# Kernel tuning notes

Hardware: AMD Instinct MI355X
Metric: run time of the kernel (lower is better)

## Reference

```python
import jax, jax.numpy as jnp
import numpy as np

# Perfect 8-ary tree, 6 levels, level-order node indexing.
K = 8            # children per internal node
D = 512          # embedding_dim
P = 8            # number of dependency types (num_params)
OFF = [0, 1, 9, 73, 585, 4681, 37449]  # level start offsets; N = 37449
N = OFF[-1]


def setup_inputs() -> dict:
    key = jax.random.key(0)
    ks = jax.random.split(key, 8)
    s = 1.0 / np.sqrt(D)  # torch default-ish init scale, avoids LSTM saturation
    return {
        "embeddings": jax.random.normal(ks[0], (N, D), dtype=jnp.float32),
        "dep_types": jax.random.randint(ks[1], (N,), 0, P, dtype=jnp.int32),
        "W_dep": jax.random.normal(ks[2], (P, D, D), dtype=jnp.float32) * s,
        "b_dep": jax.random.normal(ks[3], (P, D), dtype=jnp.float32) * s,
        "W_ih": jax.random.normal(ks[4], (4 * D, D), dtype=jnp.float32) * s,
        "W_hh": jax.random.normal(ks[5], (4 * D, D), dtype=jnp.float32) * s,
        "b_ih": jax.random.normal(ks[6], (4 * D,), dtype=jnp.float32) * s,
        "b_hh": jax.random.normal(ks[7], (4 * D,), dtype=jnp.float32) * s,
    }


def _lstm_final_c(seq, W_ih, W_hh, b_ih, b_hh):
    # seq: [B, T, D]; 1-layer LSTM with zero init state; returns final cell state c_T [B, D]
    B = seq.shape[0]
    h0 = jnp.zeros((B, D), seq.dtype)

    def step(carry, z_t):
        h, c = carry
        gates = z_t @ W_ih.T + h @ W_hh.T + b_ih + b_hh  # [B, 4D]
        i, f, g, o = jnp.split(gates, 4, axis=-1)        # torch gate order i,f,g,o
        i, f, o = jax.nn.sigmoid(i), jax.nn.sigmoid(f), jax.nn.sigmoid(o)
        g = jnp.tanh(g)
        c = f * c + i * g
        h = o * jnp.tanh(c)
        return (h, c), None

    (h, c), _ = jax.lax.scan(step, (h0, h0), jnp.swapaxes(seq, 0, 1))
    return c


def reference(embeddings, dep_types, W_dep, b_dep, W_ih, W_hh, b_ih, b_hh):
    # Leaves (level 5): LSTM over length-1 sequence [x] -> final cell state.
    leaf_x = embeddings[OFF[5]:OFF[6]]                       # [32768, D]
    z = _lstm_final_c(leaf_x[:, None, :], W_ih, W_hh, b_ih, b_hh)

    # Level-synchronous bottom-up sweep (exactly the recursion's per-node math).
    for l in range(4, -1, -1):
        m = OFF[l + 1] - OFF[l]                              # nodes at this level
        child_z = z.reshape(m, K, D)                         # children's subtree codes
        child_dep = dep_types[OFF[l + 1]:OFF[l + 2]].reshape(m, K)
        onehot = jax.nn.one_hot(child_dep, P, dtype=child_z.dtype)  # [m, K, P]
        # per-dep Linear: z_c = W_dep[dep] @ x_c + b_dep[dep]
        zc = jnp.einsum('mkj,pij,mkp->mki', child_z, W_dep, onehot) + onehot @ b_dep
        x = embeddings[OFF[l]:OFF[l + 1]]                    # node's own embedding, last in seq
        seq = jnp.concatenate([zc, x[:, None, :]], axis=1)   # [m, K+1, D]
        z = _lstm_final_c(seq, W_ih, W_hh, b_ih, b_hh)

    return z  # root sentence embedding, [1, D]
```

## Files before the change

### kernel.cpp

```cpp
#include <hip/hip_runtime.h>

typedef __attribute__((ext_vector_type(8))) short short8;
typedef __attribute__((ext_vector_type(4))) float f32x4;
typedef _Float16 half_t;

__device__ __forceinline__ unsigned short f2bf(float x){
  union { float f; unsigned u; } v; v.f = x;
  unsigned r = v.u + 0x7fffu + ((v.u >> 16) & 1u);
  return (unsigned short)(r >> 16);
}
__device__ __forceinline__ float sigm(float x){ return 1.0f / (1.0f + __expf(-x)); }
__device__ __forceinline__ float tanh_(float x){
  float e = __expf(2.0f * x);
  return 1.0f - 2.0f / (e + 1.0f);
}
__device__ __forceinline__ short8 load_bf8_f32(const float* p){
  float4 a = *(const float4*)p;
  float4 b = *(const float4*)(p + 4);
  short8 r;
  r[0]=(short)f2bf(a.x); r[1]=(short)f2bf(a.y); r[2]=(short)f2bf(a.z); r[3]=(short)f2bf(a.w);
  r[4]=(short)f2bf(b.x); r[5]=(short)f2bf(b.y); r[6]=(short)f2bf(b.z); r[7]=(short)f2bf(b.w);
  return r;
}
__device__ __forceinline__ f32x4 mfma16(short8 a, short8 b, f32x4 c){
  return __builtin_amdgcn_mfma_f32_16x16x32_bf16(a, b, c, 0, 0, 0);
}
__device__ __forceinline__ void gload16(const void* g, void* lds){
  __builtin_amdgcn_global_load_lds((const __attribute__((address_space(1))) void*)g,
                                   (__attribute__((address_space(3))) void*)lds, 16, 0, 0);
}
__device__ __forceinline__ f32x4 shfl_xor4(f32x4 v, int m){
  f32x4 r;
  r[0]=__shfl_xor(v[0],m); r[1]=__shfl_xor(v[1],m);
  r[2]=__shfl_xor(v[2],m); r[3]=__shfl_xor(v[3],m);
  return r;
}
__device__ __forceinline__ float pick4(f32x4 v, int k){
  float a = (k&1)? v[1] : v[0];
  float b = (k&1)? v[3] : v[2];
  return (k&2)? b : a;
}
__device__ __forceinline__ f32x4 sel4(f32x4 a0, f32x4 a1, f32x4 a2, f32x4 a3, int k){
  f32x4 x = (k&1)? a1 : a0;
  f32x4 y = (k&1)? a3 : a2;
  return (k&2)? y : x;
}

#define KSTAGE1(AB, BB, off)                                                         \
  {                                                                                  \
    _Pragma("unroll")                                                                \
    for (int q = 0; q < 4; ++q){                                                     \
      gload16(AB[q] + (off), As + (q*32 + w*8)*64);                                  \
      gload16(BB[q] + (off), Bs + (q*32 + w*8)*64);                                  \
    }                                                                                \
  }

#define KCOMP1                                                                       \
  {                                                                                  \
    _Pragma("unroll")                                                                \
    for (int kk = 0; kk < 2; ++kk){                                                  \
      short8 av[4], bv[4];                                                           \
      _Pragma("unroll")                                                              \
      for (int i = 0; i < 4; ++i)                                                    \
        av[i] = *(const short8*)&As[(wm*64 + i*16 + r15)*64 + (((kk*4 + g4) ^ (r15 & 7))*8)]; \
      _Pragma("unroll")                                                              \
      for (int i = 0; i < 4; ++i)                                                    \
        bv[i] = *(const short8*)&Bs[(wn*64 + i*16 + r15)*64 + (((kk*4 + g4) ^ (r15 & 7))*8)]; \
      _Pragma("unroll")                                                              \
      for (int i = 0; i < 4; ++i)                                                    \
        _Pragma("unroll")                                                            \
        for (int j = 0; j < 4; ++j) acc[i][j] = mfma16(av[i], bv[j], acc[i][j]);     \
    }                                                                                \
  }

#define KLOOP1(AB, BB)                                                               \
  for (int kt = 0; kt < 8; ++kt){                                                    \
    KSTAGE1(AB, BB, kt*64)                                                           \
    __syncthreads();                                                                 \
    KCOMP1                                                                           \
    __syncthreads();                                                                 \
  }

__global__ __launch_bounds__(256) void prep_kernel(
    const float* __restrict__ emb, const int* __restrict__ dep,
    const float* __restrict__ W_dep, const float* __restrict__ b_dep,
    const float* __restrict__ W_ih, const float* __restrict__ W_hh,
    const float* __restrict__ b_ih, const float* __restrict__ b_hh,
    unsigned short* __restrict__ embb, unsigned short* __restrict__ Wih_il,
    unsigned short* __restrict__ Whh_il, unsigned short* __restrict__ Wleaf,
    unsigned short* __restrict__ WdT, float* __restrict__ bsum, float* __restrict__ bc,
    int* __restrict__ perm, int* __restrict__ tile_p, int* __restrict__ meta)
{
  const int bid = blockIdx.x, tid = threadIdx.x;
  if (bid < 1024){
    for (size_t i = (size_t)bid*256 + tid; i < 2396736ull; i += 1024ull*256)
      *(short8*)(embb + i*8) = load_bf8_f32(emb + i*8);
  } else if (bid < 1536){
    int idx = (bid-1024)*256 + tid; int r = idx >> 6, c8 = idx & 63;
    int sr = (r & 3)*512 + (r >> 2);
    *(short8*)(Wih_il + (size_t)r*512 + c8*8) = load_bf8_f32(W_ih + (size_t)sr*512 + c8*8);
  } else if (bid < 2048){
    int idx = (bid-1536)*256 + tid; int r = idx >> 6, c8 = idx & 63;
    int sr = (r & 3)*512 + (r >> 2);
    *(short8*)(Whh_il + (size_t)r*512 + c8*8) = load_bf8_f32(W_hh + (size_t)sr*512 + c8*8);
  } else if (bid < 2304){
    int idx = (bid-2048)*256 + tid; int r = idx >> 6, c8 = idx & 63;
    int sr = ((r & 1) ? 2 : 0)*512 + (r >> 1);
    *(short8*)(Wleaf + (size_t)r*512 + c8*8) = load_bf8_f32(W_ih + (size_t)sr*512 + c8*8);
  } else if (bid < 2816){
    __shared__ unsigned short tle[64][65];
    int lb = bid - 2304; int p = lb >> 6; int tile = lb & 63;
    int i0 = (tile >> 3)*64, j0 = (tile & 7)*64;
    const float* src = W_dep + (size_t)p*512*512;
    for (int q = 0; q < 16; ++q){
      int e = q*256 + tid; int li = e >> 6, lj = e & 63;
      tle[li][lj] = f2bf(src[(size_t)(i0+li)*512 + (j0+lj)]);
    }
    __syncthreads();
    unsigned short* dst = WdT + (size_t)p*512*512;
    for (int q = 0; q < 16; ++q){
      int e = q*256 + tid; int lj = e >> 6, li = e & 63;
      dst[(size_t)(j0+lj)*512 + (i0+li)] = tle[li][lj];
    }
  } else if (bid < 2824){
    int r = (bid-2816)*256 + tid;
    if (r < 2048){ int g = r & 3, j = r >> 2; bsum[r] = b_ih[g*512+j] + b_hh[g*512+j]; }
  } else if (bid < 2888){
    __shared__ float bd[512];
    int lb = bid - 2824; int p = lb >> 3, ch = lb & 7;
    for (int i = tid; i < 512; i += 256) bd[i] = b_dep[p*512 + i];
    __syncthreads();
    int r = ch*256 + tid; int g = r & 3, j = r >> 2;
    const float* wr = W_ih + (size_t)(g*512 + j)*512;
    float s = 0.0f;
    for (int i = 0; i < 512; ++i) s = fmaf(wr[i], bd[i], s);
    bc[(size_t)p*2048 + r] = s;
  } else {
    __shared__ int cnt[8], base[8], fill[8];
    int lb = bid - 2888; const int l = lb >> 3, t = lb & 7;
    const int M_[5]  = {1,8,64,512,4096};
    const int CB_[5] = {1,9,73,585,4681};
    const int MT_[5] = {8,8,8,12,40};
    const int PB_[5] = {69632,61440,53248,40960,0};
    const int TB_[5] = {544,480,416,320,0};
    const int m = M_[l], cb = CB_[l], MT = MT_[l];
    int* pm = perm + PB_[l] + t*MT*128;
    int* tp = tile_p + TB_[l] + t*MT;
    if (tid < 8){ cnt[tid] = 0; fill[tid] = 0; }
    __syncthreads();
    for (int n = tid; n < m; n += 256) atomicAdd(&cnt[dep[cb + n*8 + t]], 1);
    __syncthreads();
    if (tid == 0){
      int tiles = 0;
      for (int p = 0; p < 8; ++p){
        base[p] = tiles*128;
        int g = (cnt[p] + 127) >> 7;
        for (int q = 0; q < g; ++q) tp[tiles + q] = p;
        tiles += g;
      }
      meta[l*8 + t] = tiles;
    }
    __syncthreads();
    for (int i = tid; i < MT*128; i += 256) pm[i] = -1;
    __syncthreads();
    for (int n = tid; n < m; n += 256){
      int p = dep[cb + n*8 + t];
      pm[base[p] + atomicAdd(&fill[p], 1)] = n;
    }
  }
}

__global__ __launch_bounds__(256) void combo_gemm(
    const unsigned short* __restrict__ A,
    const unsigned short* __restrict__ WdT,
    unsigned short* __restrict__ C)
{
  const int p  = blockIdx.x >> 6;
  const int mt = (blockIdx.x >> 2) & 15;
  const int nb = blockIdx.x & 3;
  __shared__ unsigned short As[8192];
  __shared__ unsigned short Bs[8192];
  const int tid = threadIdx.x, lane = tid & 63, w = tid >> 6;
  const int wm = w >> 1, wn = w & 1;
  const int r15 = lane & 15, g4 = lane >> 4;
  const int kc = ((lane & 7) ^ (lane >> 3)) * 8;

  const unsigned short* ab[4]; const unsigned short* bb[4];
  #pragma unroll
  for (int q = 0; q < 4; ++q){
    int rl = mt*128 + q*32 + w*8 + (lane >> 3);
    ab[q] = A + (size_t)rl*512 + kc;
    int br = nb*128 + q*32 + w*8 + (lane >> 3);
    bb[q] = WdT + (size_t)p*262144 + (size_t)br*512 + kc;
  }
  f32x4 acc[4][4] = {};
  KLOOP1(ab, bb)
  unsigned short* Cp = C + (size_t)p*1048576;
  #pragma unroll
  for (int mi = 0; mi < 4; ++mi)
    #pragma unroll
    for (int ni = 0; ni < 4; ++ni)
      #pragma unroll
      for (int j = 0; j < 4; ++j){
        int row = mt*128 + wm*64 + mi*16 + g4*4 + j;
        int col = nb*128 + wn*64 + ni*16 + r15;
        Cp[(size_t)row*512 + col] = f2bf(acc[mi][ni][j]);
      }
}

__global__ __launch_bounds__(256) void leaf_gemm(
    const unsigned short* __restrict__ embL,
    const unsigned short* __restrict__ Wleaf,
    const float* __restrict__ bsum,
    unsigned short* __restrict__ zo)
{
  const int mt = (blockIdx.x & 7)*32 + ((blockIdx.x >> 3) & 31);
  const int nb = blockIdx.x >> 8;
  __shared__ unsigned short As[8192];
  __shared__ unsigned short Bs[8192];
  const int tid = threadIdx.x, lane = tid & 63, w = tid >> 6;
  const int wm = w >> 1, wn = w & 1;
  const int r15 = lane & 15, g4 = lane >> 4;
  const int kc = ((lane & 7) ^ (lane >> 3)) * 8;

  const unsigned short* ab[4]; const unsigned short* bb[4];
  #pragma unroll
  for (int q = 0; q < 4; ++q){
    int rl = mt*128 + q*32 + w*8 + (lane >> 3);
    ab[q] = embL + (size_t)rl*512 + kc;
    int br = nb*128 + q*32 + w*8 + (lane >> 3);
    bb[q] = Wleaf + (size_t)br*512 + kc;
  }
  f32x4 acc[4][4] = {};
  KLOOP1(ab, bb)
  const int g2 = r15 & 1;
  #pragma unroll
  for (int ni = 0; ni < 4; ++ni){
    int ci = nb*128 + wn*64 + ni*16 + r15;
    float b = bsum[4*(ci >> 1) + (g2 ? 2 : 0)];
    #pragma unroll
    for (int mi = 0; mi < 4; ++mi){
      acc[mi][ni][0]+=b; acc[mi][ni][1]+=b; acc[mi][ni][2]+=b; acc[mi][ni][3]+=b;
    }
  }
  #pragma unroll
  for (int mi = 0; mi < 4; ++mi)
    #pragma unroll
    for (int ni = 0; ni < 4; ++ni){
      f32x4 a0 = acc[mi][ni];
      f32x4 a1 = shfl_xor4(a0, 1);
      f32x4 vi_ = g2 ? a1 : a0;
      f32x4 vg_ = g2 ? a0 : a1;
      int jz = (nb*128 + wn*64 + ni*16 + r15) >> 1;
      #pragma unroll
      for (int u = 0; u < 2; ++u){
        int jrow = (g2 << 1) + u;
        float zi = pick4(vi_, jrow), zg = pick4(vg_, jrow);
        int row = mt*128 + wm*64 + mi*16 + g4*4 + jrow;
        zo[(size_t)row*512 + jz] = f2bf(sigm(zi) * tanh_(zg));
      }
    }
}

__device__ __forceinline__ void step_core(
    unsigned short* As, unsigned short* Bs,
    const unsigned short* __restrict__ embb,
    const unsigned short* __restrict__ Wcombo,
    const unsigned short* __restrict__ Wih_il,
    const unsigned short* __restrict__ Whh_il,
    const float* __restrict__ bsum, const float* __restrict__ bc,
    const unsigned short* __restrict__ zin, unsigned short* __restrict__ zo,
    const unsigned short* __restrict__ hi, unsigned short* __restrict__ ho,
    float* __restrict__ cbuf, float* __restrict__ outp,
    const int* __restrict__ pm, const int* __restrict__ tp,
    int node_base, int m, int t, int mt, int nbq, int l)
{
  const int tid = threadIdx.x, lane = tid & 63, w = tid >> 6;
  const int wm = w >> 1, wn = w & 1;
  const int r15 = lane & 15, g4 = lane >> 4;
  const int kc = ((lane & 7) ^ (lane >> 3)) * 8;
  const int first = (t == 0), last = (t == 8);
  const int p = tp ? tp[mt] : 0;

  int nn[4];
  #pragma unroll
  for (int q = 0; q < 4; ++q){
    int rl = mt*128 + q*32 + w*8 + (lane >> 3);
    int n = pm ? pm[rl] : (rl < m ? rl : -1);
    nn[q] = (n < 0) ? 0 : n;
  }
  f32x4 acc[4][4] = {};
  {
    const unsigned short* Bx = (t < 8) ? (Wcombo + (size_t)p*1048576) : Wih_il;
    const unsigned short* ab[4]; const unsigned short* bb[4];
    #pragma unroll
    for (int q = 0; q < 4; ++q){
      ab[q] = (t < 8) ? (zin + ((size_t)nn[q]*8 + t)*512 + kc)
                      : (embb + (size_t)(node_base + nn[q])*512 + kc);
      int br = nbq*128 + q*32 + w*8 + (lane >> 3);
      bb[q] = Bx + (size_t)br*512 + kc;
    }
    KLOOP1(ab, bb)
  }
  if (!first){
    const unsigned short* ab[4]; const unsigned short* bb[4];
    #pragma unroll
    for (int q = 0; q < 4; ++q){
      ab[q] = hi + (size_t)nn[q]*512 + kc;
      int br = nbq*128 + q*32 + w*8 + (lane >> 3);
      bb[q] = Whh_il + (size_t)br*512 + kc;
    }
    KLOOP1(ab, bb)
  }
  const int gate = r15 & 3;
  #pragma unroll
  for (int ni = 0; ni < 4; ++ni){
    int ci = nbq*128 + wn*64 + ni*16 + r15;
    float b = bsum[ci] + ((t < 8) ? bc[(size_t)p*2048 + ci] : 0.0f);
    #pragma unroll
    for (int mi = 0; mi < 4; ++mi){
      acc[mi][ni][0]+=b; acc[mi][ni][1]+=b; acc[mi][ni][2]+=b; acc[mi][ni][3]+=b;
    }
  }
  const int jr = r15 & 3;
  #pragma unroll
  for (int mi = 0; mi < 4; ++mi){
    int rl = mt*128 + wm*64 + mi*16 + g4*4 + jr;
    int n = pm ? pm[rl] : (rl < m ? rl : -1);
    #pragma unroll
    for (int ni = 0; ni < 4; ++ni){
      f32x4 a0 = acc[mi][ni];
      f32x4 a1 = shfl_xor4(a0, 1);
      f32x4 a2 = shfl_xor4(a0, 2);
      f32x4 a3 = shfl_xor4(a1, 2);
      f32x4 vi_ = sel4(a0,a1,a2,a3, gate);
      f32x4 vf_ = sel4(a0,a1,a2,a3, gate^1);
      f32x4 vg_ = sel4(a0,a1,a2,a3, gate^2);
      f32x4 vo_ = sel4(a0,a1,a2,a3, gate^3);
      float xi = pick4(vi_, jr), xf = pick4(vf_, jr);
      float xg = pick4(vg_, jr), xo = pick4(vo_, jr);
      if (n >= 0){
        int jz = nbq*32 + wn*16 + ni*4 + (r15 >> 2);
        size_t idx = (size_t)n*512 + jz;
        float i_ = sigm(xi), f_ = sigm(xf), g_ = tanh_(xg), o_ = sigm(xo);
        float cold = first ? 0.0f : cbuf[idx];
        float cn = fmaf(f_, cold, i_*g_);
        if (!last){ cbuf[idx] = cn; ho[idx] = f2bf(o_*tanh_(cn)); }
        else { if (l > 0) zo[idx] = f2bf(cn); else outp[idx] = cn; }
      }
    }
  }
}

__global__ __launch_bounds__(256) void step_kernel(
    const unsigned short* __restrict__ embb,
    const unsigned short* __restrict__ Wcombo,
    const unsigned short* __restrict__ Wih_il,
    const unsigned short* __restrict__ Whh_il,
    const float* __restrict__ bsum, const float* __restrict__ bc,
    const unsigned short* __restrict__ zin, unsigned short* __restrict__ zo,
    const unsigned short* __restrict__ hi, unsigned short* __restrict__ ho,
    float* __restrict__ cbuf, float* __restrict__ outp,
    const int* __restrict__ perm_t, const int* __restrict__ tile_t,
    const int* __restrict__ meta_t,
    int fixed_nt, int MTcap, int node_base, int m, int t, int l)
{
  __shared__ unsigned short As[8192];
  __shared__ unsigned short Bs[8192];
  int ntiles = meta_t ? *meta_t : fixed_nt;
  if (ntiles > MTcap) ntiles = MTcap;
  const int njobs = ntiles * 16;
  const int chunk = (njobs + 7) >> 3;
  const int g = blockIdx.x & 7, i = blockIdx.x >> 3;
  const int job = g*chunk + i;
  if (i >= chunk || job >= njobs) return;
  const int mt = job % ntiles, nbq = job / ntiles;
  step_core(As, Bs, embb, Wcombo, Wih_il, Whh_il, bsum, bc, zin, zo, hi, ho,
            cbuf, outp, perm_t, tile_t, node_base, m, t, mt, nbq, l);
}

__global__ __launch_bounds__(256) void gatex_kernel(
    const unsigned short* __restrict__ embb,
    const unsigned short* __restrict__ Wcombo,
    const unsigned short* __restrict__ Wih_il,
    const float* __restrict__ bsum, const float* __restrict__ bc,
    const unsigned short* __restrict__ zin,
    half_t* __restrict__ gx, unsigned short* __restrict__ h0out,
    float* __restrict__ cbuf,
    const int* __restrict__ perm_l, const int* __restrict__ tile_l,
    const int* __restrict__ meta_l,
    int MT, int m, int node_base)
{
  __shared__ unsigned short As[8192];
  __shared__ unsigned short Bs[8192];
  const int jt = blockIdx.x >> 4, nbq = blockIdx.x & 15;
  int t, mt, p = 0;
  const int* pm = nullptr;
  if (jt < 8*MT){
    t = jt / MT; mt = jt - t*MT;
    if (mt >= meta_l[t]) return;
    pm = perm_l + t*MT*128;
    p = tile_l[t*MT + mt];
  } else {
    t = 8; mt = jt - 8*MT;
  }
  const int tid = threadIdx.x, lane = tid & 63, w = tid >> 6;
  const int wm = w >> 1, wn = w & 1;
  const int r15 = lane & 15, g4 = lane >> 4;
  const int kc = ((lane & 7) ^ (lane >> 3)) * 8;

  int nn[4];
  #pragma unroll
  for (int q = 0; q < 4; ++q){
    int rl = mt*128 + q*32 + w*8 + (lane >> 3);
    int n = pm ? pm[rl] : (rl < m ? rl : -1);
    nn[q] = (n < 0) ? 0 : n;
  }
  const unsigned short* Bx = (t < 8) ? (Wcombo + (size_t)p*1048576) : Wih_il;
  const unsigned short* ab[4]; const unsigned short* bb[4];
  #pragma unroll
  for (int q = 0; q < 4; ++q){
    ab[q] = (t < 8) ? (zin + ((size_t)nn[q]*8 + t)*512 + kc)
                    : (embb + (size_t)(node_base + nn[q])*512 + kc);
    int br = nbq*128 + q*32 + w*8 + (lane >> 3);
    bb[q] = Bx + (size_t)br*512 + kc;
  }
  f32x4 acc[4][4] = {};
  KLOOP1(ab, bb)

  #pragma unroll
  for (int ni = 0; ni < 4; ++ni){
    int ci = nbq*128 + wn*64 + ni*16 + r15;
    float b = bsum[ci] + ((t < 8) ? bc[(size_t)p*2048 + ci] : 0.0f);
    #pragma unroll
    for (int mi = 0; mi < 4; ++mi){
      acc[mi][ni][0]+=b; acc[mi][ni][1]+=b; acc[mi][ni][2]+=b; acc[mi][ni][3]+=b;
    }
  }

  if (t == 0){
    const int gate = r15 & 3;
    const int jr = r15 & 3;
    #pragma unroll
    for (int mi = 0; mi < 4; ++mi){
      int rl = mt*128 + wm*64 + mi*16 + g4*4 + jr;
      int n = pm ? pm[rl] : (rl < m ? rl : -1);
      #pragma unroll
      for (int ni = 0; ni < 4; ++ni){
        f32x4 a0 = acc[mi][ni];
        f32x4 a1 = shfl_xor4(a0, 1);
        f32x4 a2 = shfl_xor4(a0, 2);
        f32x4 a3 = shfl_xor4(a1, 2);
        f32x4 vi_ = sel4(a0,a1,a2,a3, gate);
        f32x4 vg_ = sel4(a0,a1,a2,a3, gate^2);
        f32x4 vo_ = sel4(a0,a1,a2,a3, gate^3);
        float xi = pick4(vi_, jr);
        float xg = pick4(vg_, jr);
        float xo = pick4(vo_, jr);
        if (n >= 0){
          int jz = nbq*32 + wn*16 + ni*4 + (r15 >> 2);
          size_t idx = (size_t)n*512 + jz;
          float cn = sigm(xi) * tanh_(xg);
          cbuf[idx] = cn;
          h0out[idx] = f2bf(sigm(xo) * tanh_(cn));
        }
      }
    }
  } else {
    #pragma unroll
    for (int mi = 0; mi < 4; ++mi)
      #pragma unroll
      for (int ni = 0; ni < 4; ++ni){
        int ci = nbq*128 + wn*64 + ni*16 + r15;
        #pragma unroll
        for (int j = 0; j < 4; ++j){
          int rl = mt*128 + wm*64 + mi*16 + g4*4 + j;
          int n = pm ? pm[rl] : (rl < m ? rl : -1);
          if (n >= 0) gx[((size_t)t*m + n)*2048 + ci] = (half_t)acc[mi][ni][j];
        }
      }
  }
}

__global__ __launch_bounds__(256) void hstep_kernel(
    const unsigned short* __restrict__ Whh_il,
    const half_t* __restrict__ gx,
    const unsigned short* __restrict__ hi, unsigned short* __restrict__ ho,
    float* __restrict__ cbuf,
    unsigned short* __restrict__ zo, float* __restrict__ outp,
    int m, int t, int last)
{
  __shared__ unsigned short As[8192];
  __shared__ unsigned short Bs[8192];
  const int mt = blockIdx.x >> 4, nbq = blockIdx.x & 15;
  const int tid = threadIdx.x, lane = tid & 63, w = tid >> 6;
  const int wm = w >> 1, wn = w & 1;
  const int r15 = lane & 15, g4 = lane >> 4;
  const int kc = ((lane & 7) ^ (lane >> 3)) * 8;

  int nn[4];
  #pragma unroll
  for (int q = 0; q < 4; ++q){
    int rl = mt*128 + q*32 + w*8 + (lane >> 3);
    nn[q] = (rl < m) ? rl : 0;
  }
  const unsigned short* ab[4]; const unsigned short* bb[4];
  #pragma unroll
  for (int q = 0; q < 4; ++q){
    ab[q] = hi + (size_t)nn[q]*512 + kc;
    int br = nbq*128 + q*32 + w*8 + (lane >> 3);
    bb[q] = Whh_il + (size_t)br*512 + kc;
  }
  f32x4 acc[4][4] = {};
  KLOOP1(ab, bb)

  #pragma unroll
  for (int mi = 0; mi < 4; ++mi)
    #pragma unroll
    for (int ni = 0; ni < 4; ++ni){
      int ci = nbq*128 + wn*64 + ni*16 + r15;
      #pragma unroll
      for (int j = 0; j < 4; ++j){
        int rl = mt*128 + wm*64 + mi*16 + g4*4 + j;
        if (rl < m) acc[mi][ni][j] += (float)gx[((size_t)t*m + rl)*2048 + ci];
      }
    }

  const int gate = r15 & 3;
  const int jr = r15 & 3;
  #pragma unroll
  for (int mi = 0; mi < 4; ++mi){
    int rl = mt*128 + wm*64 + mi*16 + g4*4 + jr;
    int n = (rl < m) ? rl : -1;
    #pragma unroll
    for (int ni = 0; ni < 4; ++ni){
      f32x4 a0 = acc[mi][ni];
      f32x4 a1 = shfl_xor4(a0, 1);
      f32x4 a2 = shfl_xor4(a0, 2);
      f32x4 a3 = shfl_xor4(a1, 2);
      f32x4 vi_ = sel4(a0,a1,a2,a3, gate);
      f32x4 vf_ = sel4(a0,a1,a2,a3, gate^1);
      f32x4 vg_ = sel4(a0,a1,a2,a3, gate^2);
      f32x4 vo_ = sel4(a0,a1,a2,a3, gate^3);
      float xi = pick4(vi_, jr), xf = pick4(vf_, jr);
      float xg = pick4(vg_, jr), xo = pick4(vo_, jr);
      if (n >= 0){
        int jz = nbq*32 + wn*16 + ni*4 + (r15 >> 2);
        size_t idx = (size_t)n*512 + jz;
        float i_ = sigm(xi), f_ = sigm(xf), g_ = tanh_(xg), o_ = sigm(xo);
        float cn = fmaf(f_, cbuf[idx], i_*g_);
        if (!last){ cbuf[idx] = cn; ho[idx] = f2bf(o_*tanh_(cn)); }
        else { if (zo) zo[idx] = f2bf(cn); else outp[idx] = cn; }
      }
    }
  }
}

extern "C" void kernel_launch(void* const* d_in, const int* in_sizes, int n_in,
                              void* d_out, int out_size, void* d_ws, size_t ws_size,
                              hipStream_t stream)
{
  (void)in_sizes; (void)n_in; (void)out_size; (void)ws_size;
  const float* emb   = (const float*)d_in[0];
  const int*   dep   = (const int*)  d_in[1];
  const float* W_dep = (const float*)d_in[2];
  const float* b_dep = (const float*)d_in[3];
  const float* W_ih  = (const float*)d_in[4];
  const float* W_hh  = (const float*)d_in[5];
  const float* b_ih  = (const float*)d_in[6];
  const float* b_hh  = (const float*)d_in[7];
  float* out = (float*)d_out;

  unsigned short* embb   = (unsigned short*)d_ws;
  unsigned short* Wih_il = embb   + 19173888ull;
  unsigned short* Whh_il = Wih_il + 1048576ull;
  unsigned short* Wleaf  = Whh_il + 1048576ull;
  unsigned short* WdT    = Wleaf  + 524288ull;
  unsigned short* Wcombo = WdT    + 2097152ull;
  unsigned short* Z0     = Wcombo + 8388608ull;
  unsigned short* Z1     = Z0     + 16777216ull;
  unsigned short* hA     = Z1     + 2097152ull;
  unsigned short* hB     = hA     + 2097152ull;
  float* cbuf  = (float*)(hB + 2097152ull);
  float* bsum  = cbuf + 2097152ull;
  float* bc    = bsum + 2048;
  int*  perm   = (int*)(bc + 16384);
  int*  tile_p = perm + 77824;
  int*  meta   = tile_p + 608;
  half_t* gx   = (half_t*)(meta + 40);

  prep_kernel<<<2928, 256, 0, stream>>>(emb, dep, W_dep, b_dep, W_ih, W_hh, b_ih, b_hh,
                                        embb, Wih_il, Whh_il, Wleaf, WdT, bsum, bc,
                                        perm, tile_p, meta);
  combo_gemm<<<512, 256, 0, stream>>>(Wih_il, WdT, Wcombo);
  leaf_gemm<<<2048, 256, 0, stream>>>(embb + (size_t)4681*512, Wleaf, bsum, Z0);

  for (int t = 0; t <= 8; ++t){
    const unsigned short* hi = (t & 1) ? hA : hB;
    unsigned short* ho       = (t & 1) ? hB : hA;
    int grid = (t < 8) ? 40*16 : 32*16;
    step_kernel<<<grid, 256, 0, stream>>>(
        embb, Wcombo, Wih_il, Whh_il, bsum, bc,
        Z0, Z1, hi, ho, cbuf, nullptr,
        (t < 8) ? (perm + t*40*128) : nullptr,
        (t < 8) ? (tile_p + t*40) : nullptr,
        (t < 8) ? (meta + 4*8 + t) : nullptr,
        32, 40, 585, 4096, t, 4);
  }

  struct LvP { int m, MT, PB, TB, nb_, mtiles; };
  const LvP LP[4] = {
    {512, 12, 40960, 320, 73, 4},
    {64,  8,  53248, 416, 9,  1},
    {8,   8,  61440, 480, 1,  1},
    {1,   8,  69632, 544, 0,  1}};
  for (int k = 0; k < 4; ++k){
    const int l = 3 - k;
    const unsigned short* zin = (l & 1) ? Z1 : Z0;
    unsigned short* zo        = (l & 1) ? Z0 : Z1;
    gatex_kernel<<<(8*LP[k].MT + LP[k].mtiles)*16, 256, 0, stream>>>(
        embb, Wcombo, Wih_il, bsum, bc, zin, gx, hA, cbuf,
        perm + LP[k].PB, tile_p + LP[k].TB, meta + l*8,
        LP[k].MT, LP[k].m, LP[k].nb_);
    for (int t = 1; t <= 8; ++t){
      const unsigned short* hi = (t & 1) ? hA : hB;
      unsigned short* ho       = (t & 1) ? hB : hA;
      hstep_kernel<<<LP[k].mtiles*16, 256, 0, stream>>>(
          Whh_il, gx, hi, ho, cbuf,
          (l > 0) ? zo : nullptr, (l == 0) ? out : nullptr,
          LP[k].m, t, (t == 8));
    }
  }
}
```

Before: 1.407 ms.

## Fuse small-level launches with persistent grid-barrier chain and GEMV gate kernel

Merges the combo and leaf GEMMs into one launch. For the three smallest tree levels, it replaces the tiled gatex kernel and eight per-step hstep launches with a GEMV-style gatex_small kernel and one persistent 16-block hchain kernel. That kernel loops over the timesteps and syncs through an atomic counter barrier that prep_kernel resets. The aim is to cut launch overhead and tile waste on levels with 1–64 nodes. In exchange it relies on all 16 blocks being co-resident for the spin barrier, and the GEMV path re-reads weights for every node pair.

```diff
diff --git a/kernel.cpp b/kernel.cpp
--- a/kernel.cpp
+++ b/kernel.cpp
@@ -8,6 +8,9 @@
   union { float f; unsigned u; } v; v.f = x;
   unsigned r = v.u + 0x7fffu + ((v.u >> 16) & 1u);
   return (unsigned short)(r >> 16);
+}
+__device__ __forceinline__ float bf2f(unsigned short u){
+  union { float f; unsigned x; } v; v.x = ((unsigned)u) << 16; return v.f;
 }
 __device__ __forceinline__ float sigm(float x){ return 1.0f / (1.0f + __expf(-x)); }
 __device__ __forceinline__ float tanh_(float x){
@@ -44,6 +47,18 @@
   f32x4 x = (k&1)? a1 : a0;
   f32x4 y = (k&1)? a3 : a2;
   return (k&2)? y : x;
+}
+
+__device__ __forceinline__ void chainbar(int* ctr, int target){
+  __syncthreads();
+  if (threadIdx.x == 0){
+    __threadfence();
+    __hip_atomic_fetch_add(ctr, 1, __ATOMIC_RELEASE, __HIP_MEMORY_SCOPE_AGENT);
+    while (__hip_atomic_load(ctr, __ATOMIC_RELAXED, __HIP_MEMORY_SCOPE_AGENT) < target)
+      __builtin_amdgcn_s_sleep(2);
+    (void)__hip_atomic_load(ctr, __ATOMIC_ACQUIRE, __HIP_MEMORY_SCOPE_AGENT);
+  }
+  __syncthreads();
 }
 
 #define KSTAGE1(AB, BB, off)                                                         \
@@ -89,7 +104,8 @@
     unsigned short* __restrict__ embb, unsigned short* __restrict__ Wih_il,
     unsigned short* __restrict__ Whh_il, unsigned short* __restrict__ Wleaf,
     unsigned short* __restrict__ WdT, float* __restrict__ bsum, float* __restrict__ bc,
-    int* __restrict__ perm, int* __restrict__ tile_p, int* __restrict__ meta)
+    int* __restrict__ perm, int* __restrict__ tile_p, int* __restrict__ meta,
+    int* __restrict__ ctr)
 {
   const int bid = blockIdx.x, tid = threadIdx.x;
   if (bid < 1024){
@@ -135,7 +151,7 @@
     float s = 0.0f;
     for (int i = 0; i < 512; ++i) s = fmaf(wr[i], bd[i], s);
     bc[(size_t)p*2048 + r] = s;
-  } else {
+  } else if (bid < 2928){
     __shared__ int cnt[8], base[8], fill[8];
     int lb = bid - 2888; const int l = lb >> 3, t = lb & 7;
     const int M_[5]  = {1,8,64,512,4096};
@@ -167,17 +183,20 @@
       int p = dep[cb + n*8 + t];
       pm[base[p] + atomicAdd(&fill[p], 1)] = n;
     }
-  }
-}
-
-__global__ __launch_bounds__(256) void combo_gemm(
-    const unsigned short* __restrict__ A,
+  } else {
+    if (tid < 4) ctr[tid] = 0;
+  }
+}
+
+__global__ __launch_bounds__(256) void comboleaf_kernel(
+    const unsigned short* __restrict__ Wih_il,
     const unsigned short* __restrict__ WdT,
-    unsigned short* __restrict__ C)
+    unsigned short* __restrict__ Wcombo,
+    const unsigned short* __restrict__ embL,
+    const unsigned short* __restrict__ Wleaf,
+    const float* __restrict__ bsum,
+    unsigned short* __restrict__ zo)
 {
-  const int p  = blockIdx.x >> 6;
-  const int mt = (blockIdx.x >> 2) & 15;
-  const int nb = blockIdx.x & 3;
   __shared__ unsigned short As[8192];
   __shared__ unsigned short Bs[8192];
   const int tid = threadIdx.x, lane = tid & 63, w = tid >> 6;
@@ -185,81 +204,73 @@
   const int r15 = lane & 15, g4 = lane >> 4;
   const int kc = ((lane & 7) ^ (lane >> 3)) * 8;
 
-  const unsigned short* ab[4]; const unsigned short* bb[4];
-  #pragma unroll
-  for (int q = 0; q < 4; ++q){
-    int rl = mt*128 + q*32 + w*8 + (lane >> 3);
-    ab[q] = A + (size_t)rl*512 + kc;
-    int br = nb*128 + q*32 + w*8 + (lane >> 3);
-    bb[q] = WdT + (size_t)p*262144 + (size_t)br*512 + kc;
-  }
-  f32x4 acc[4][4] = {};
-  KLOOP1(ab, bb)
-  unsigned short* Cp = C + (size_t)p*1048576;
-  #pragma unroll
-  for (int mi = 0; mi < 4; ++mi)
-    #pragma unroll
-    for (int ni = 0; ni < 4; ++ni)
+  if (blockIdx.x < 512){
+    const int p  = blockIdx.x >> 6;
+    const int mt = (blockIdx.x >> 2) & 15;
+    const int nb = blockIdx.x & 3;
+    const unsigned short* ab[4]; const unsigned short* bb[4];
+    #pragma unroll
+    for (int q = 0; q < 4; ++q){
+      int rl = mt*128 + q*32 + w*8 + (lane >> 3);
+      ab[q] = Wih_il + (size_t)rl*512 + kc;
+      int br = nb*128 + q*32 + w*8 + (lane >> 3);
+      bb[q] = WdT + (size_t)p*262144 + (size_t)br*512 + kc;
+    }
+    f32x4 acc[4][4] = {};
+    KLOOP1(ab, bb)
+    unsigned short* Cp = Wcombo + (size_t)p*1048576;
+    #pragma unroll
+    for (int mi = 0; mi < 4; ++mi)
       #pragma unroll
-      for (int j = 0; j < 4; ++j){
-        int row = mt*128 + wm*64 + mi*16 + g4*4 + j;
-        int col = nb*128 + wn*64 + ni*16 + r15;
-        Cp[(size_t)row*512 + col] = f2bf(acc[mi][ni][j]);
-      }
-}
-
-__global__ __launch_bounds__(256) void leaf_gemm(
-    const unsigned short* __restrict__ embL,
-    const unsigned short* __restrict__ Wleaf,
-    const float* __restrict__ bsum,
-    unsigned short* __restrict__ zo)
-{
-  const int mt = (blockIdx.x & 7)*32 + ((blockIdx.x >> 3) & 31);
-  const int nb = blockIdx.x >> 8;
-  __shared__ unsigned short As[8192];
-  __shared__ unsigned short Bs[8192];
-  const int tid = threadIdx.x, lane = tid & 63, w = tid >> 6;
-  const int wm = w >> 1, wn = w & 1;
-  const int r15 = lane & 15, g4 = lane >> 4;
-  const int kc = ((lane & 7) ^ (lane >> 3)) * 8;
-
-  const unsigned short* ab[4]; const unsigned short* bb[4];
-  #pragma unroll
-  for (int q = 0; q < 4; ++q){
-    int rl = mt*128 + q*32 + w*8 + (lane >> 3);
-    ab[q] = embL + (size_t)rl*512 + kc;
-    int br = nb*128 + q*32 + w*8 + (lane >> 3);
-    bb[q] = Wleaf + (size_t)br*512 + kc;
-  }
-  f32x4 acc[4][4] = {};
-  KLOOP1(ab, bb)
-  const int g2 = r15 & 1;
-  #pragma unroll
-  for (int ni = 0; ni < 4; ++ni){
-    int ci = nb*128 + wn*64 + ni*16 + r15;
-    float b = bsum[4*(ci >> 1) + (g2 ? 2 : 0)];
-    #pragma unroll
-    for (int mi = 0; mi < 4; ++mi){
-      acc[mi][ni][0]+=b; acc[mi][ni][1]+=b; acc[mi][ni][2]+=b; acc[mi][ni][3]+=b;
-    }
-  }
-  #pragma unroll
-  for (int mi = 0; mi < 4; ++mi)
+      for (int ni = 0; ni < 4; ++ni)
+        #pragma unroll
+        for (int j = 0; j < 4; ++j){
+          int row = mt*128 + wm*64 + mi*16 + g4*4 + j;
+          int col = nb*128 + wn*64 + ni*16 + r15;
+          Cp[(size_t)row*512 + col] = f2bf(acc[mi][ni][j]);
+        }
+  } else {
+    const int lj = blockIdx.x - 512;
+    const int mt = (lj & 7)*32 + ((lj >> 3) & 31);
+    const int nb = lj >> 8;
+    const unsigned short* ab[4]; const unsigned short* bb[4];
+    #pragma unroll
+    for (int q = 0; q < 4; ++q){
+      int rl = mt*128 + q*32 + w*8 + (lane >> 3);
+      ab[q] = embL + (size_t)rl*512 + kc;
+      int br = nb*128 + q*32 + w*8 + (lane >> 3);
+      bb[q] = Wleaf + (size_t)br*512 + kc;
+    }
+    f32x4 acc[4][4] = {};
+    KLOOP1(ab, bb)
+    const int g2 = r15 & 1;
     #pragma unroll
     for (int ni = 0; ni < 4; ++ni){
-      f32x4 a0 = acc[mi][ni];
-      f32x4 a1 = shfl_xor4(a0, 1);
-      f32x4 vi_ = g2 ? a1 : a0;
-      f32x4 vg_ = g2 ? a0 : a1;
-      int jz = (nb*128 + wn*64 + ni*16 + r15) >> 1;
+      int ci = nb*128 + wn*64 + ni*16 + r15;
+      float b = bsum[4*(ci >> 1) + (g2 ? 2 : 0)];
       #pragma unroll
-      for (int u = 0; u < 2; ++u){
-        int jrow = (g2 << 1) + u;
-        float zi = pick4(vi_, jrow), zg = pick4(vg_, jrow);
-        int row = mt*128 + wm*64 + mi*16 + g4*4 + jrow;
-        zo[(size_t)row*512 + jz] = f2bf(sigm(zi) * tanh_(zg));
-      }
-    }
+      for (int mi = 0; mi < 4; ++mi){
+        acc[mi][ni][0]+=b; acc[mi][ni][1]+=b; acc[mi][ni][2]+=b; acc[mi][ni][3]+=b;
+      }
+    }
+    #pragma unroll
+    for (int mi = 0; mi < 4; ++mi)
+      #pragma unroll
+      for (int ni = 0; ni < 4; ++ni){
+        f32x4 a0 = acc[mi][ni];
+        f32x4 a1 = shfl_xor4(a0, 1);
+        f32x4 vi_ = g2 ? a1 : a0;
+        f32x4 vg_ = g2 ? a0 : a1;
+        int jz = (nb*128 + wn*64 + ni*16 + r15) >> 1;
+        #pragma unroll
+        for (int u = 0; u < 2; ++u){
+          int jrow = (g2 << 1) + u;
+          float zi = pick4(vi_, jrow), zg = pick4(vg_, jrow);
+          int row = mt*128 + wm*64 + mi*16 + g4*4 + jrow;
+          zo[(size_t)row*512 + jz] = f2bf(sigm(zi) * tanh_(zg));
+        }
+      }
+  }
 }
 
 __device__ __forceinline__ void step_core(
@@ -482,6 +493,97 @@
   }
 }
 
+__global__ __launch_bounds__(256) void gatex_small(
+    const unsigned short* __restrict__ embb,
+    const unsigned short* __restrict__ Wcombo,
+    const unsigned short* __restrict__ Wih_il,
+    const float* __restrict__ bsum, const float* __restrict__ bc,
+    const int* __restrict__ dep,
+    const unsigned short* __restrict__ zin,
+    half_t* __restrict__ gx, unsigned short* __restrict__ h0out,
+    float* __restrict__ cbuf,
+    int m, int node_base, int child_base)
+{
+  const int t = blockIdx.x >> 4, cb = blockIdx.x & 15;
+  const int tid = threadIdx.x;
+  const int ci = cb*128 + (tid >> 1);
+  const int kh = (tid & 1) * 256;
+  __shared__ float zf[2][512];
+  __shared__ float gl[2][128];
+
+  for (int n0 = 0; n0 < m; n0 += 2){
+    const int n1 = (n0 + 1 < m) ? n0 + 1 : n0;
+    __syncthreads();
+    for (int i = tid; i < 1024; i += 256){
+      int s = i >> 9, k = i & 511;
+      int nn = s ? n1 : n0;
+      const unsigned short* ar = (t < 8) ? (zin + ((size_t)nn*8 + t)*512)
+                                         : (embb + (size_t)(node_base + nn)*512);
+      zf[s][k] = bf2f(ar[k]);
+    }
+    __syncthreads();
+    int p0 = 0, p1 = 0;
+    if (t < 8){
+      p0 = dep[child_base + n0*8 + t];
+      p1 = dep[child_base + n1*8 + t];
+    }
+    const unsigned short* w0 = ((t < 8) ? (Wcombo + (size_t)p0*1048576) : Wih_il)
+                               + (size_t)ci*512 + kh;
+    const unsigned short* w1 = ((t < 8) ? (Wcombo + (size_t)p1*1048576) : Wih_il)
+                               + (size_t)ci*512 + kh;
+    float s0 = 0.f, s1 = 0.f;
+    if (p0 == p1){
+      for (int q = 0; q < 32; ++q){
+        short8 wv = *(const short8*)(w0 + q*8);
+        #pragma unroll
+        for (int e = 0; e < 8; ++e){
+          float wf = bf2f((unsigned short)wv[e]);
+          s0 = fmaf(wf, zf[0][kh + q*8 + e], s0);
+          s1 = fmaf(wf, zf[1][kh + q*8 + e], s1);
+        }
+      }
+    } else {
+      for (int q = 0; q < 32; ++q){
+        short8 wa = *(const short8*)(w0 + q*8);
+        short8 wb = *(const short8*)(w1 + q*8);
+        #pragma unroll
+        for (int e = 0; e < 8; ++e){
+          s0 = fmaf(bf2f((unsigned short)wa[e]), zf[0][kh + q*8 + e], s0);
+          s1 = fmaf(bf2f((unsigned short)wb[e]), zf[1][kh + q*8 + e], s1);
+        }
+      }
+    }
+    s0 += __shfl_xor(s0, 1);
+    s1 += __shfl_xor(s1, 1);
+    if ((tid & 1) == 0){
+      float b = bsum[ci];
+      float g0 = s0 + b + ((t < 8) ? bc[(size_t)p0*2048 + ci] : 0.f);
+      float g1 = s1 + b + ((t < 8) ? bc[(size_t)p1*2048 + ci] : 0.f);
+      if (t == 0){
+        gl[0][ci & 127] = g0;
+        gl[1][ci & 127] = g1;
+      } else {
+        gx[((size_t)t*m + n0)*2048 + ci] = (half_t)g0;
+        if (n1 != n0) gx[((size_t)t*m + n1)*2048 + ci] = (half_t)g1;
+      }
+    }
+    if (t == 0){
+      __syncthreads();
+      if (tid < 64){
+        int s = tid >> 5, j = tid & 31;
+        int nn = s ? n1 : n0;
+        if (!(s && n1 == n0)){
+          float gi = gl[s][4*j], gg = gl[s][4*j + 2], go = gl[s][4*j + 3];
+          float c = sigm(gi) * tanh_(gg);
+          size_t idx = (size_t)nn*512 + cb*32 + j;
+          cbuf[idx] = c;
+          h0out[idx] = f2bf(sigm(go) * tanh_(c));
+        }
+      }
+    }
+  }
+}
+
 __global__ __launch_bounds__(256) void hstep_kernel(
     const unsigned short* __restrict__ Whh_il,
     const half_t* __restrict__ gx,
@@ -556,6 +658,88 @@
   }
 }
 
+__global__ __launch_bounds__(256) void hchain_kernel(
+    const unsigned short* __restrict__ Whh_il,
+    const half_t* __restrict__ gx,
+    unsigned short* __restrict__ hA, unsigned short* __restrict__ hB,
+    float* __restrict__ cbuf,
+    unsigned short* __restrict__ zo, float* __restrict__ outp,
+    int m, int* __restrict__ ctr)
+{
+  __shared__ unsigned short As[8192];
+  __shared__ unsigned short Bs[8192];
+  const int mt = blockIdx.x >> 4, nbq = blockIdx.x & 15;
+  const int tid = threadIdx.x, lane = tid & 63, w = tid >> 6;
+  const int wm = w >> 1, wn = w & 1;
+  const int r15 = lane & 15, g4 = lane >> 4;
+  const int kc = ((lane & 7) ^ (lane >> 3)) * 8;
+  const int gate = r15 & 3;
+  const int jr = r15 & 3;
+
+  int nn[4];
+  #pragma unroll
+  for (int q = 0; q < 4; ++q){
+    int rl = mt*128 + q*32 + w*8 + (lane >> 3);
+    nn[q] = (rl < m) ? rl : 0;
+  }
+
+  for (int t = 1; t <= 8; ++t){
+    const int last = (t == 8);
+    const unsigned short* hi = (t & 1) ? hA : hB;
+    unsigned short* ho       = (t & 1) ? hB : hA;
+
+    const unsigned short* ab[4]; const unsigned short* bb[4];
+    #pragma unroll
+    for (int q = 0; q < 4; ++q){
+      ab[q] = hi + (size_t)nn[q]*512 + kc;
+      int br = nbq*128 + q*32 + w*8 + (lane >> 3);
+      bb[q] = Whh_il + (size_t)br*512 + kc;
+    }
+    f32x4 acc[4][4] = {};
+    KLOOP1(ab, bb)
+
+    #pragma unroll
+    for (int mi = 0; mi < 4; ++mi)
+      #pragma unroll
+      for (int ni = 0; ni < 4; ++ni){
+        int ci = nbq*128 + wn*64 + ni*16 + r15;
+        #pragma unroll
+        for (int j = 0; j < 4; ++j){
+          int rl = mt*128 + wm*64 + mi*16 + g4*4 + j;
+          if (rl < m) acc[mi][ni][j] += (float)gx[((size_t)t*m + rl)*2048 + ci];
+        }
+      }
+
+    #pragma unroll
+    for (int mi = 0; mi < 4; ++mi){
+      int rl = mt*128 + wm*64 + mi*16 + g4*4 + jr;
+      int n = (rl < m) ? rl : -1;
+      #pragma unroll
+      for (int ni = 0; ni < 4; ++ni){
+        f32x4 a0 = acc[mi][ni];
+        f32x4 a1 = shfl_xor4(a0, 1);
+        f32x4 a2 = shfl_xor4(a0, 2);
+        f32x4 a3 = shfl_xor4(a1, 2);
+        f32x4 vi_ = sel4(a0,a1,a2,a3, gate);
+        f32x4 vf_ = sel4(a0,a1,a2,a3, gate^1);
+        f32x4 vg_ = sel4(a0,a1,a2,a3, gate^2);
+        f32x4 vo_ = sel4(a0,a1,a2,a3, gate^3);
+        float xi = pick4(vi_, jr), xf = pick4(vf_, jr);
+        float xg = pick4(vg_, jr), xo = pick4(vo_, jr);
+        if (n >= 0){
+          int jz = nbq*32 + wn*16 + ni*4 + (r15 >> 2);
+          size_t idx = (size_t)n*512 + jz;
+          float i_ = sigm(xi), f_ = sigm(xf), g_ = tanh_(xg), o_ = sigm(xo);
+          float cn = fmaf(f_, cbuf[idx], i_*g_);
+          if (!last){ cbuf[idx] = cn; ho[idx] = f2bf(o_*tanh_(cn)); }
+          else { if (zo) zo[idx] = f2bf(cn); else outp[idx] = cn; }
+        }
+      }
+    }
+    if (!last) chainbar(ctr, gridDim.x * t);
+  }
+}
+
 extern "C" void kernel_launch(void* const* d_in, const int* in_sizes, int n_in,
                               void* d_out, int out_size, void* d_ws, size_t ws_size,
                               hipStream_t stream)
@@ -587,13 +771,14 @@
   int*  perm   = (int*)(bc + 16384);
   int*  tile_p = perm + 77824;
   int*  meta   = tile_p + 608;
-  half_t* gx   = (half_t*)(meta + 40);
-
-  prep_kernel<<<2928, 256, 0, stream>>>(emb, dep, W_dep, b_dep, W_ih, W_hh, b_ih, b_hh,
+  int*  ctr    = meta + 40;
+  half_t* gx   = (half_t*)(ctr + 4);
+
+  prep_kernel<<<2929, 256, 0, stream>>>(emb, dep, W_dep, b_dep, W_ih, W_hh, b_ih, b_hh,
                                         embb, Wih_il, Whh_il, Wleaf, WdT, bsum, bc,
-                                        perm, tile_p, meta);
-  combo_gemm<<<512, 256, 0, stream>>>(Wih_il, WdT, Wcombo);
-  leaf_gemm<<<2048, 256, 0, stream>>>(embb + (size_t)4681*512, Wleaf, bsum, Z0);
+                                        perm, tile_p, meta, ctr);
+  comboleaf_kernel<<<2560, 256, 0, stream>>>(Wih_il, WdT, Wcombo,
+                                             embb + (size_t)4681*512, Wleaf, bsum, Z0);
 
   for (int t = 0; t <= 8; ++t){
     const unsigned short* hi = (t & 1) ? hA : hB;
@@ -608,27 +793,29 @@
         32, 40, 585, 4096, t, 4);
   }
 
-  struct LvP { int m, MT, PB, TB, nb_, mtiles; };
-  const LvP LP[4] = {
-    {512, 12, 40960, 320, 73, 4},
-    {64,  8,  53248, 416, 9,  1},
-    {8,   8,  61440, 480, 1,  1},
-    {1,   8,  69632, 544, 0,  1}};
-  for (int k = 0; k < 4; ++k){
-    const int l = 3 - k;
+  gatex_kernel<<<(8*12 + 4)*16, 256, 0, stream>>>(
+      embb, Wcombo, Wih_il, bsum, bc, Z1, gx, hA, cbuf,
+      perm + 40960, tile_p + 320, meta + 3*8, 12, 512, 73);
+  for (int t = 1; t <= 8; ++t){
+    const unsigned short* hi = (t & 1) ? hA : hB;
+    unsigned short* ho       = (t & 1) ? hB : hA;
+    hstep_kernel<<<4*16, 256, 0, stream>>>(
+        Whh_il, gx, hi, ho, cbuf,
+        (t == 8) ? Z0 : nullptr, nullptr, 512, t, (t == 8));
+  }
+
+  struct LvS { int m, nb_, cb_; };
+  const LvS LS[3] = { {64, 9, 73}, {8, 1, 9}, {1, 0, 1} };
+  for (int k = 0; k < 3; ++k){
+    const int l = 2 - k;
     const unsigned short* zin = (l & 1) ? Z1 : Z0;
     unsigned short* zo        = (l & 1) ? Z0 : Z1;
-    gatex_kernel<<<(8*LP[k].MT + LP[k].mtiles)*16, 256, 0, stream>>>(
-        embb, Wcombo, Wih_il, bsum, bc, zin, gx, hA, cbuf,
-        perm + LP[k].PB, tile_p + LP[k].TB, meta + l*8,
-        LP[k].MT, LP[k].m, LP[k].nb_);
-    for (int t = 1; t <= 8; ++t){
-      const unsigned short* hi = (t & 1) ? hA : hB;
-      unsigned short* ho       = (t & 1) ? hB : hA;
-      hstep_kernel<<<LP[k].mtiles*16, 256, 0, stream>>>(
-          Whh_il, gx, hi, ho, cbuf,
-          (l > 0) ? zo : nullptr, (l == 0) ? out : nullptr,
-          LP[k].m, t, (t == 8));
-    }
-  }
-}
+    gatex_small<<<144, 256, 0, stream>>>(
+        embb, Wcombo, Wih_il, bsum, bc, dep, zin, gx, hA, cbuf,
+        LS[k].m, LS[k].nb_, LS[k].cb_);
+    hchain_kernel<<<16, 256, 0, stream>>>(
+        Whh_il, gx, hA, hB, cbuf,
+        (l > 0) ? zo : nullptr, (l == 0) ? out : nullptr,
+        LS[k].m, ctr + k);
+  }
+}
```

Result: slower. 1.735 ms (+23.3%).
